# Performance work log

Measured on AMD Instinct MI355X. Metric: run time of the kernel, lower is better.

## Reference

```python
import jax, jax.numpy as jnp
import numpy as np

N_NODES = 50000
N_EDGES = 800000
D_IN, D_HID, D_OUT = 64, 128, 64


def _glorot(key, fan_in, fan_out):
    lim = (6.0 / (fan_in + fan_out)) ** 0.5
    return jax.random.uniform(key, (fan_in, fan_out), jnp.float32, -lim, lim)


def setup_inputs() -> dict:
    key = jax.random.key(0)
    ks = jax.random.split(key, 10)
    x = jax.random.normal(ks[0], (N_NODES, D_IN), jnp.float32)
    edge_index = jax.random.randint(ks[1], (2, N_EDGES), 0, N_NODES, jnp.int64)
    # GINConv1 MLP: Linear(D_IN->D_HID), ReLU, Linear(D_HID->D_HID)
    W1a = _glorot(ks[2], D_IN, D_HID); b1a = jnp.zeros((D_HID,), jnp.float32)
    W1b = _glorot(ks[3], D_HID, D_HID); b1b = jnp.zeros((D_HID,), jnp.float32)
    # GINConv2 MLP: Linear(D_HID->D_HID), ReLU, Linear(D_HID->D_OUT)
    W2a = _glorot(ks[4], D_HID, D_HID); b2a = jnp.zeros((D_HID,), jnp.float32)
    W2b = _glorot(ks[5], D_HID, D_OUT); b2b = jnp.zeros((D_OUT,), jnp.float32)
    return {"x": x, "edge_index": edge_index,
            "W1a": W1a, "b1a": b1a, "W1b": W1b, "b1b": b1b,
            "W2a": W2a, "b2a": b2a, "W2b": W2b, "b2b": b2b}


def _gin_conv(x, src, dst, Wa, ba, Wb, bb):
    # GIN aggregation (eps = 0): h_i = x_i + sum_{j in N(i)} x_j
    msgs = x[src]                                   # [E, d] gather
    agg = jax.ops.segment_sum(msgs, dst, num_segments=x.shape[0])  # [N, d]
    h = x + agg
    # 2-layer MLP
    h = jax.nn.relu(h @ Wa + ba)
    return h @ Wb + bb


def reference(x, edge_index, W1a, b1a, W1b, b1b, W2a, b2a, W2b, b2b):
    src, dst = edge_index[0], edge_index[1]
    h = jax.nn.relu(_gin_conv(x, src, dst, W1a, b1a, W1b, b1b))
    h = jax.nn.relu(_gin_conv(h, src, dst, W2a, b2a, W2b, b2b))
    return h
```

## Files before the change

kernel.cpp:

```cpp
#include <hip/hip_runtime.h>

#define N_NODES 50000
#define N_EDGES 800000
#define N_SG 8
#define DST_PER_SG (N_NODES / N_SG)

typedef __attribute__((ext_vector_type(8))) short short8;
typedef __attribute__((ext_vector_type(4))) float floatx4;

static __device__ __forceinline__ unsigned short f2b(float f) {
    unsigned int u = __float_as_uint(f);
    unsigned int r = u + 0x7fffu + ((u >> 16) & 1u);
    return (unsigned short)(r >> 16);
}
static __device__ __forceinline__ unsigned int pk(float a, float b) {
    return (unsigned)f2b(a) | ((unsigned)f2b(b) << 16);
}
static __device__ __forceinline__ float blo(unsigned int u) {
    return __uint_as_float(u << 16);
}
static __device__ __forceinline__ float bhi(unsigned int u) {
    return __uint_as_float(u & 0xffff0000u);
}

__global__ __launch_bounds__(256) void hist_part_kernel(
    const int* __restrict__ dst, int* __restrict__ deg, int n) {
    const int sg = blockIdx.x & (N_SG - 1);
    const int cb = blockIdx.x >> 3;
    const int nchunks = gridDim.x >> 3;
    const int chunk = (n + nchunks - 1) / nchunks;
    const int lo = cb * chunk;
    const int hi = min(lo + chunk, n);
    const int dlo = sg * DST_PER_SG, dhi = dlo + DST_PER_SG;
    for (int e = lo + threadIdx.x; e < hi; e += 256) {
        const int d = dst[e];
        if (d >= dlo && d < dhi) atomicAdd(&deg[d], 1);
    }
}

__global__ __launch_bounds__(1024) void scanA_kernel(
    const int* __restrict__ deg, int* __restrict__ bsum, int n) {
    __shared__ int s[1024];
    const int tid = threadIdx.x;
    int i = blockIdx.x * 1024 + tid;
    s[tid] = (i < n) ? deg[i] : 0;
    __syncthreads();
    for (int d = 512; d > 0; d >>= 1) {
        if (tid < d) s[tid] += s[tid + d];
        __syncthreads();
    }
    if (tid == 0) bsum[blockIdx.x] = s[0];
}

__global__ __launch_bounds__(1024) void scanC_kernel(
    const int* __restrict__ deg, const int* __restrict__ bsum,
    int* __restrict__ off, int* __restrict__ cursor, int n) {
    __shared__ int s[1024];
    __shared__ int bpref;
    const int tid = threadIdx.x;
    if (tid == 0) {
        int p = 0;
        for (int j = 0; j < blockIdx.x; ++j) p += bsum[j];
        bpref = p;
    }
    const int i = blockIdx.x * 1024 + tid;
    const int v = (i < n) ? deg[i] : 0;
    s[tid] = v;
    __syncthreads();
    for (int d = 1; d < 1024; d <<= 1) {
        int t = (tid >= d) ? s[tid - d] : 0;
        __syncthreads();
        s[tid] += t;
        __syncthreads();
    }
    const int excl = s[tid] - v + bpref;
    if (i < n) {
        off[i] = excl;
        cursor[i] = excl;
        if (i == n - 1) off[n] = excl + v;
    }
}

__global__ __launch_bounds__(256) void fill_part_kernel(
    const int* __restrict__ src, const int* __restrict__ dst,
    int* __restrict__ cursor, unsigned short* __restrict__ nbr, int n) {
    const int sg = blockIdx.x & (N_SG - 1);
    const int cb = blockIdx.x >> 3;
    const int nchunks = gridDim.x >> 3;
    const int chunk = (n + nchunks - 1) / nchunks;
    const int lo = cb * chunk;
    const int hi = min(lo + chunk, n);
    const int dlo = sg * DST_PER_SG, dhi = dlo + DST_PER_SG;
    for (int e = lo + threadIdx.x; e < hi; e += 256) {
        const int d = dst[e];
        if (d >= dlo && d < dhi) {
            int pos = atomicAdd(&cursor[d], 1);
            nbr[pos] = (unsigned short)src[e];
        }
    }
}

__global__ __launch_bounds__(256) void prep_kernel(
    const float* __restrict__ W1a, const float* __restrict__ W1b,
    const float* __restrict__ W2a, const float* __restrict__ W2b,
    const float* __restrict__ x, unsigned short* __restrict__ W1aT,
    unsigned short* __restrict__ W1bT, unsigned short* __restrict__ W2aT,
    unsigned short* __restrict__ W2bT, unsigned short* __restrict__ xb) {
    int i = blockIdx.x * 256 + threadIdx.x;
    if (i < 8192) {
        int n = i >> 6, k = i & 63;
        W1aT[i] = f2b(W1a[k * 128 + n]);
    } else if (i < 24576) {
        int j = i - 8192, n = j >> 7, k = j & 127;
        W1bT[j] = f2b(W1b[k * 128 + n]);
    } else if (i < 40960) {
        int j = i - 24576, n = j >> 7, k = j & 127;
        W2aT[j] = f2b(W2a[k * 128 + n]);
    } else if (i < 49152) {
        int j = i - 40960, n = j >> 7, k = j & 127;
        W2bT[j] = f2b(W2b[k * 64 + n]);
    } else {
        int j = i - 49152;
        if (j < N_NODES * 16) {
            float4 v = ((const float4*)x)[j];
            uint2 o;
            o.x = pk(v.x, v.y);
            o.y = pk(v.z, v.w);
            ((uint2*)xb)[j] = o;
        }
    }
}

__global__ __launch_bounds__(256) void gather1_kernel(
    const unsigned short* __restrict__ xb, const int* __restrict__ off,
    const unsigned short* __restrict__ nbr, unsigned short* __restrict__ t1,
    int n_nodes) {
    const int tid = threadIdx.x;
    const int node = blockIdx.x * 16 + (tid >> 4);
    const int c = tid & 15;
    if (node >= n_nodes) return;
    const uint2* xr = (const uint2*)xb;
    const uint2 a = xr[(size_t)node * 16 + c];
    float f0 = blo(a.x), f1 = bhi(a.x), f2 = blo(a.y), f3 = bhi(a.y);
    const int lo = off[node], hi = off[node + 1];
    int j = lo;
    for (; j + 4 <= hi; j += 4) {
        const int s0 = nbr[j], s1 = nbr[j + 1], s2 = nbr[j + 2],
                  s3 = nbr[j + 3];
        const uint2 v0 = xr[(size_t)s0 * 16 + c];
        const uint2 v1 = xr[(size_t)s1 * 16 + c];
        const uint2 v2 = xr[(size_t)s2 * 16 + c];
        const uint2 v3 = xr[(size_t)s3 * 16 + c];
        f0 += (blo(v0.x) + blo(v1.x)) + (blo(v2.x) + blo(v3.x));
        f1 += (bhi(v0.x) + bhi(v1.x)) + (bhi(v2.x) + bhi(v3.x));
        f2 += (blo(v0.y) + blo(v1.y)) + (blo(v2.y) + blo(v3.y));
        f3 += (bhi(v0.y) + bhi(v1.y)) + (bhi(v2.y) + bhi(v3.y));
    }
    for (; j < hi; ++j) {
        const uint2 v = xr[(size_t)nbr[j] * 16 + c];
        f0 += blo(v.x); f1 += bhi(v.x);
        f2 += blo(v.y); f3 += bhi(v.y);
    }
    uint2 o;
    o.x = pk(f0, f1);
    o.y = pk(f2, f3);
    ((uint2*)t1)[(size_t)node * 16 + c] = o;
}

__global__ __launch_bounds__(256) void gather2_kernel(
    const unsigned short* __restrict__ h, const int* __restrict__ off,
    const unsigned short* __restrict__ nbr, unsigned short* __restrict__ t2,
    int n_nodes) {
    const int tid = threadIdx.x;
    const int node = blockIdx.x * 16 + (tid >> 4);
    const int c = tid & 15;
    if (node >= n_nodes) return;
    const uint4* hr = (const uint4*)h;
    const uint4 a = hr[(size_t)node * 16 + c];
    float f0 = blo(a.x), f1 = bhi(a.x), f2 = blo(a.y), f3 = bhi(a.y);
    float f4 = blo(a.z), f5 = bhi(a.z), f6 = blo(a.w), f7 = bhi(a.w);
    const int lo = off[node], hi = off[node + 1];
    int j = lo;
    for (; j + 4 <= hi; j += 4) {
        const int s0 = nbr[j], s1 = nbr[j + 1], s2 = nbr[j + 2],
                  s3 = nbr[j + 3];
        const uint4 v0 = hr[(size_t)s0 * 16 + c];
        const uint4 v1 = hr[(size_t)s1 * 16 + c];
        const uint4 v2 = hr[(size_t)s2 * 16 + c];
        const uint4 v3 = hr[(size_t)s3 * 16 + c];
        f0 += (blo(v0.x) + blo(v1.x)) + (blo(v2.x) + blo(v3.x));
        f1 += (bhi(v0.x) + bhi(v1.x)) + (bhi(v2.x) + bhi(v3.x));
        f2 += (blo(v0.y) + blo(v1.y)) + (blo(v2.y) + blo(v3.y));
        f3 += (bhi(v0.y) + bhi(v1.y)) + (bhi(v2.y) + bhi(v3.y));
        f4 += (blo(v0.z) + blo(v1.z)) + (blo(v2.z) + blo(v3.z));
        f5 += (bhi(v0.z) + bhi(v1.z)) + (bhi(v2.z) + bhi(v3.z));
        f6 += (blo(v0.w) + blo(v1.w)) + (blo(v2.w) + blo(v3.w));
        f7 += (bhi(v0.w) + bhi(v1.w)) + (bhi(v2.w) + bhi(v3.w));
    }
    for (; j < hi; ++j) {
        const uint4 v = hr[(size_t)nbr[j] * 16 + c];
        f0 += blo(v.x); f1 += bhi(v.x); f2 += blo(v.y); f3 += bhi(v.y);
        f4 += blo(v.z); f5 += bhi(v.z); f6 += blo(v.w); f7 += bhi(v.w);
    }
    uint4 o;
    o.x = pk(f0, f1); o.y = pk(f2, f3);
    o.z = pk(f4, f5); o.w = pk(f6, f7);
    ((uint4*)t2)[(size_t)node * 16 + c] = o;
}

template <int DIN, int DH, int DOUT, bool OUT_BF16>
__global__ __launch_bounds__(256) void mlp_mfma_kernel(
    const unsigned short* __restrict__ t, const unsigned short* __restrict__ WaT,
    const float* __restrict__ ba, const unsigned short* __restrict__ WbT,
    const float* __restrict__ bb, void* __restrict__ outp, int n_rows) {
    constexpr int SA = DIN + 16;
    constexpr int SH = DH + 16;
    __shared__ unsigned short tA[64 * SA];
    __shared__ unsigned short hidA[64 * SH];

    const int tid = threadIdx.x;
    const int row0 = blockIdx.x * 64;

    constexpr int CHUNKS = 64 * DIN / 8;
    const uint4* tg = (const uint4*)t;
    for (int i = tid; i < CHUNKS; i += 256) {
        const int row = i / (DIN / 8);
        const int cb = i % (DIN / 8);
        uint4 v = {0u, 0u, 0u, 0u};
        const int gr = row0 + row;
        if (gr < n_rows) v = tg[(size_t)gr * (DIN / 8) + cb];
        *(uint4*)&tA[row * SA + cb * 8] = v;
    }
    __syncthreads();

    const int lane = tid & 63;
    const int wv = tid >> 6;
    const int quad = lane >> 4;
    const int l16 = lane & 15;
    const int m0 = wv * 16;

    short8 a1[DIN / 32];
#pragma unroll
    for (int kk = 0; kk < DIN / 32; ++kk)
        a1[kk] = *(const short8*)&tA[(m0 + l16) * SA + kk * 32 + quad * 8];
#pragma unroll
    for (int nt = 0; nt < DH / 16; ++nt) {
        floatx4 acc = {0.f, 0.f, 0.f, 0.f};
#pragma unroll
        for (int kk = 0; kk < DIN / 32; ++kk) {
            short8 b =
                *(const short8*)&WaT[(nt * 16 + l16) * DIN + kk * 32 + quad * 8];
            acc = __builtin_amdgcn_mfma_f32_16x16x32_bf16(a1[kk], b, acc, 0, 0, 0);
        }
        const float bias = ba[nt * 16 + l16];
#pragma unroll
        for (int r = 0; r < 4; ++r) {
            const float v = fmaxf(acc[r] + bias, 0.f);
            hidA[(m0 + quad * 4 + r) * SH + nt * 16 + l16] = f2b(v);
        }
    }

    short8 a2[DH / 32];
#pragma unroll
    for (int kk = 0; kk < DH / 32; ++kk)
        a2[kk] = *(const short8*)&hidA[(m0 + l16) * SH + kk * 32 + quad * 8];
#pragma unroll
    for (int nt = 0; nt < DOUT / 16; ++nt) {
        floatx4 acc = {0.f, 0.f, 0.f, 0.f};
#pragma unroll
        for (int kk = 0; kk < DH / 32; ++kk) {
            short8 b =
                *(const short8*)&WbT[(nt * 16 + l16) * DH + kk * 32 + quad * 8];
            acc = __builtin_amdgcn_mfma_f32_16x16x32_bf16(a2[kk], b, acc, 0, 0, 0);
        }
        const float bias = bb[nt * 16 + l16];
#pragma unroll
        for (int r = 0; r < 4; ++r) {
            const float v = fmaxf(acc[r] + bias, 0.f);
            const int grow = row0 + m0 + quad * 4 + r;
            if (grow < n_rows) {
                if (OUT_BF16)
                    ((unsigned short*)outp)[(size_t)grow * DOUT + nt * 16 + l16] =
                        f2b(v);
                else
                    ((float*)outp)[(size_t)grow * DOUT + nt * 16 + l16] = v;
            }
        }
    }
}

extern "C" void kernel_launch(void* const* d_in, const int* in_sizes, int n_in,
                              void* d_out, int out_size, void* d_ws,
                              size_t ws_size, hipStream_t stream) {
    const float* x   = (const float*)d_in[0];
    const int*   ei  = (const int*)d_in[1];
    const float* W1a = (const float*)d_in[2];
    const float* b1a = (const float*)d_in[3];
    const float* W1b = (const float*)d_in[4];
    const float* b1b = (const float*)d_in[5];
    const float* W2a = (const float*)d_in[6];
    const float* b2a = (const float*)d_in[7];
    const float* W2b = (const float*)d_in[8];
    const float* b2b = (const float*)d_in[9];
    float* out = (float*)d_out;

    const int* src = ei;
    const int* dst = ei + N_EDGES;

    unsigned short* xb = (unsigned short*)d_ws;
    unsigned short* t1 = xb + (size_t)N_NODES * 64;
    unsigned short* h  = t1 + (size_t)N_NODES * 64;
    unsigned short* t2 = h + (size_t)N_NODES * 128;
    unsigned short* W1aT = t2 + (size_t)N_NODES * 128;
    unsigned short* W1bT = W1aT + 8192;
    unsigned short* W2aT = W1bT + 16384;
    unsigned short* W2bT = W2aT + 16384;
    int* deg    = (int*)(W2bT + 8192);
    int* off    = deg + N_NODES;
    int* cursor = off + N_NODES + 1;
    int* bsum   = cursor + N_NODES;
    unsigned short* nbr = (unsigned short*)(bsum + 64);

    constexpr int NB = (N_NODES + 1023) / 1024;

    hipMemsetAsync(deg, 0, N_NODES * sizeof(int), stream);
    hist_part_kernel<<<1024, 256, 0, stream>>>(dst, deg, N_EDGES);
    scanA_kernel<<<NB, 1024, 0, stream>>>(deg, bsum, N_NODES);
    scanC_kernel<<<NB, 1024, 0, stream>>>(deg, bsum, off, cursor, N_NODES);
    fill_part_kernel<<<1024, 256, 0, stream>>>(src, dst, cursor, nbr, N_EDGES);
    prep_kernel<<<(49152 + N_NODES * 16 + 255) / 256, 256, 0, stream>>>(
        W1a, W1b, W2a, W2b, x, W1aT, W1bT, W2aT, W2bT, xb);

    gather1_kernel<<<(N_NODES + 15) / 16, 256, 0, stream>>>(xb, off, nbr, t1,
                                                            N_NODES);
    mlp_mfma_kernel<64, 128, 128, true>
        <<<(N_NODES + 63) / 64, 256, 0, stream>>>(t1, W1aT, b1a, W1bT, b1b, h,
                                                  N_NODES);

    gather2_kernel<<<(N_NODES + 15) / 16, 256, 0, stream>>>(h, off, nbr, t2,
                                                            N_NODES);
    mlp_mfma_kernel<128, 128, 64, false>
        <<<(N_NODES + 63) / 64, 256, 0, stream>>>(t2, W2aT, b2a, W2bT, b2b, out,
                                                  N_NODES);
}
```

Measured before the change: 267.1 us.

## Build CSR with per-edge atomic ranks instead of partitioned cursor fill

Replaces the destination-partitioned histogram and fill passes, which each read all edges once per subgroup, with a single histogram pass that records each edge's atomic rank. Those ranks are then combined with the scan offsets in an atomic-free fill pass. The degree memset is folded into the prep kernel, which removes one launch. The cost is an extra 3.2 MB rank buffer and random-address atomics that are no longer localized per subgroup, and the neighbor order is still nondeterministic.

```diff
diff --git a/kernel.cpp b/kernel.cpp
--- a/kernel.cpp
+++ b/kernel.cpp
@@ -2,8 +2,6 @@
 
 #define N_NODES 50000
 #define N_EDGES 800000
-#define N_SG 8
-#define DST_PER_SG (N_NODES / N_SG)
 
 typedef __attribute__((ext_vector_type(8))) short short8;
 typedef __attribute__((ext_vector_type(4))) float floatx4;
@@ -23,19 +21,11 @@
     return __uint_as_float(u & 0xffff0000u);
 }
 
-__global__ __launch_bounds__(256) void hist_part_kernel(
-    const int* __restrict__ dst, int* __restrict__ deg, int n) {
-    const int sg = blockIdx.x & (N_SG - 1);
-    const int cb = blockIdx.x >> 3;
-    const int nchunks = gridDim.x >> 3;
-    const int chunk = (n + nchunks - 1) / nchunks;
-    const int lo = cb * chunk;
-    const int hi = min(lo + chunk, n);
-    const int dlo = sg * DST_PER_SG, dhi = dlo + DST_PER_SG;
-    for (int e = lo + threadIdx.x; e < hi; e += 256) {
-        const int d = dst[e];
-        if (d >= dlo && d < dhi) atomicAdd(&deg[d], 1);
-    }
+__global__ void hist_rank_kernel(const int* __restrict__ dst,
+                                 int* __restrict__ deg, int* __restrict__ rank,
+                                 int n) {
+    int i = blockIdx.x * blockDim.x + threadIdx.x;
+    if (i < n) rank[i] = atomicAdd(&deg[dst[i]], 1);
 }
 
 __global__ __launch_bounds__(1024) void scanA_kernel(
@@ -54,7 +44,7 @@
 
 __global__ __launch_bounds__(1024) void scanC_kernel(
     const int* __restrict__ deg, const int* __restrict__ bsum,
-    int* __restrict__ off, int* __restrict__ cursor, int n) {
+    int* __restrict__ off, int n) {
     __shared__ int s[1024];
     __shared__ int bpref;
     const int tid = threadIdx.x;
@@ -76,28 +66,17 @@
     const int excl = s[tid] - v + bpref;
     if (i < n) {
         off[i] = excl;
-        cursor[i] = excl;
         if (i == n - 1) off[n] = excl + v;
     }
 }
 
-__global__ __launch_bounds__(256) void fill_part_kernel(
-    const int* __restrict__ src, const int* __restrict__ dst,
-    int* __restrict__ cursor, unsigned short* __restrict__ nbr, int n) {
-    const int sg = blockIdx.x & (N_SG - 1);
-    const int cb = blockIdx.x >> 3;
-    const int nchunks = gridDim.x >> 3;
-    const int chunk = (n + nchunks - 1) / nchunks;
-    const int lo = cb * chunk;
-    const int hi = min(lo + chunk, n);
-    const int dlo = sg * DST_PER_SG, dhi = dlo + DST_PER_SG;
-    for (int e = lo + threadIdx.x; e < hi; e += 256) {
-        const int d = dst[e];
-        if (d >= dlo && d < dhi) {
-            int pos = atomicAdd(&cursor[d], 1);
-            nbr[pos] = (unsigned short)src[e];
-        }
-    }
+__global__ void fill_kernel(const int* __restrict__ src,
+                            const int* __restrict__ dst,
+                            const int* __restrict__ rank,
+                            const int* __restrict__ off,
+                            unsigned short* __restrict__ nbr, int n) {
+    int i = blockIdx.x * blockDim.x + threadIdx.x;
+    if (i < n) nbr[off[dst[i]] + rank[i]] = (unsigned short)src[i];
 }
 
 __global__ __launch_bounds__(256) void prep_kernel(
@@ -105,7 +84,8 @@
     const float* __restrict__ W2a, const float* __restrict__ W2b,
     const float* __restrict__ x, unsigned short* __restrict__ W1aT,
     unsigned short* __restrict__ W1bT, unsigned short* __restrict__ W2aT,
-    unsigned short* __restrict__ W2bT, unsigned short* __restrict__ xb) {
+    unsigned short* __restrict__ W2bT, unsigned short* __restrict__ xb,
+    int* __restrict__ deg) {
     int i = blockIdx.x * 256 + threadIdx.x;
     if (i < 8192) {
         int n = i >> 6, k = i & 63;
@@ -119,15 +99,16 @@
     } else if (i < 49152) {
         int j = i - 40960, n = j >> 7, k = j & 127;
         W2bT[j] = f2b(W2b[k * 64 + n]);
+    } else if (i < 49152 + N_NODES * 16) {
+        int j = i - 49152;
+        float4 v = ((const float4*)x)[j];
+        uint2 o;
+        o.x = pk(v.x, v.y);
+        o.y = pk(v.z, v.w);
+        ((uint2*)xb)[j] = o;
     } else {
-        int j = i - 49152;
-        if (j < N_NODES * 16) {
-            float4 v = ((const float4*)x)[j];
-            uint2 o;
-            o.x = pk(v.x, v.y);
-            o.y = pk(v.z, v.w);
-            ((uint2*)xb)[j] = o;
-        }
+        int j = i - (49152 + N_NODES * 16);
+        if (j < N_NODES) deg[j] = 0;
     }
 }
 
@@ -315,21 +296,24 @@
     unsigned short* W1bT = W1aT + 8192;
     unsigned short* W2aT = W1bT + 16384;
     unsigned short* W2bT = W2aT + 16384;
-    int* deg    = (int*)(W2bT + 8192);
-    int* off    = deg + N_NODES;
-    int* cursor = off + N_NODES + 1;
-    int* bsum   = cursor + N_NODES;
-    unsigned short* nbr = (unsigned short*)(bsum + 64);
+    int* deg  = (int*)(W2bT + 8192);
+    int* off  = deg + N_NODES;
+    int* bsum = off + N_NODES + 1;
+    int* rank = bsum + 64;
+    unsigned short* nbr = (unsigned short*)(rank + N_EDGES);
 
     constexpr int NB = (N_NODES + 1023) / 1024;
-
-    hipMemsetAsync(deg, 0, N_NODES * sizeof(int), stream);
-    hist_part_kernel<<<1024, 256, 0, stream>>>(dst, deg, N_EDGES);
+    constexpr int PREP_THREADS = 49152 + N_NODES * 16 + N_NODES;
+
+    prep_kernel<<<(PREP_THREADS + 255) / 256, 256, 0, stream>>>(
+        W1a, W1b, W2a, W2b, x, W1aT, W1bT, W2aT, W2bT, xb, deg);
+
+    hist_rank_kernel<<<(N_EDGES + 255) / 256, 256, 0, stream>>>(dst, deg, rank,
+                                                                N_EDGES);
     scanA_kernel<<<NB, 1024, 0, stream>>>(deg, bsum, N_NODES);
-    scanC_kernel<<<NB, 1024, 0, stream>>>(deg, bsum, off, cursor, N_NODES);
-    fill_part_kernel<<<1024, 256, 0, stream>>>(src, dst, cursor, nbr, N_EDGES);
-    prep_kernel<<<(49152 + N_NODES * 16 + 255) / 256, 256, 0, stream>>>(
-        W1a, W1b, W2a, W2b, x, W1aT, W1bT, W2aT, W2bT, xb);
+    scanC_kernel<<<NB, 1024, 0, stream>>>(deg, bsum, off, N_NODES);
+    fill_kernel<<<(N_EDGES + 255) / 256, 256, 0, stream>>>(src, dst, rank, off,
+                                                           nbr, N_EDGES);
 
     gather1_kernel<<<(N_NODES + 15) / 16, 256, 0, stream>>>(xb, off, nbr, t1,
                                                             N_NODES);
```

Result: faster. 239.0 us (-10.5%).
